# Optimization experiments

Measured on AMD Instinct MI355X. Metric: run time of the kernel, lower is better.

Reference implementation:

```python
import jax, jax.numpy as jnp
import numpy as np

B, S, H, KVH, D, MD = 4, 4096, 2, 1, 2, 5  # batch, seq, heads, kv heads, head_dim, model_dim
EPS, SCALE = 1e-6, 16.0


def _rmsnorm(t):
    # RMSNormNoWeight with scale=16.0 over last dim
    var = jnp.mean(t * t, axis=-1, keepdims=True)
    return SCALE * t * jax.lax.rsqrt(var + EPS)


def _rope(t, cos, sin):
    # t: (B, S, h, D); cos/sin: (S, D//2). Complex multiply on interleaved pairs.
    tr, ti = t[..., 0::2], t[..., 1::2]
    c = cos[None, :, None, :]
    s = sin[None, :, None, :]
    out_r = tr * c - ti * s
    out_i = tr * s + ti * c
    return jnp.stack([out_r, out_i], axis=-1).reshape(t.shape)


def setup_inputs() -> dict:
    key = jax.random.key(0)
    ks = jax.random.split(key, 9)
    return {
        "x": jax.random.normal(ks[0], (B, S, MD), jnp.float32),
        "freqs": jax.random.normal(ks[1], (S, D // 2), jnp.float32),
        "shared_qk_v": jax.random.normal(ks[2], (MD,), jnp.float32),
        "shared_v_v": jax.random.normal(ks[3], (MD,), jnp.float32),
        "shared_o_v": jax.random.normal(ks[4], (H * D,), jnp.float32),
        "shared_vproj_u": jax.random.normal(ks[5], (KVH * D,), jnp.float32),
        "q_u": jax.random.normal(ks[6], (H * D,), jnp.float32),
        "k_u": jax.random.normal(ks[7], (KVH * D,), jnp.float32),
        "o_u": jax.random.normal(ks[8], (MD,), jnp.float32),
    }


def reference(x, freqs, shared_qk_v, shared_v_v, shared_o_v, shared_vproj_u, q_u, k_u, o_u):
    b, s = x.shape[0], x.shape[1]
    # rank-1 projections: (x . v) outer u
    s_qk = jnp.sum(x * shared_qk_v, axis=-1, keepdims=True)  # (B,S,1) shared by q and k
    q = (s_qk * q_u).reshape(b, s, H, D)
    k = (s_qk * k_u).reshape(b, s, KVH, D)
    s_v = jnp.sum(x * shared_v_v, axis=-1, keepdims=True)
    v = (s_v * shared_vproj_u).reshape(b, s, KVH, D)
    # qk-norm + rotary
    q = _rmsnorm(q)
    k = _rmsnorm(k)
    cos, sin = jnp.cos(freqs), jnp.sin(freqs)
    q = _rope(q, cos, sin)
    k = _rope(k, cos, sin)
    # (B,h,S,D)
    q = q.transpose(0, 2, 1, 3)
    k = k.transpose(0, 2, 1, 3)
    v = v.transpose(0, 2, 1, 3)
    # GQA repeat kv heads
    k = jnp.repeat(k, H // KVH, axis=1)
    v = jnp.repeat(v, H // KVH, axis=1)
    scores = jnp.einsum('bhqd,bhkd->bhqk', q, k) / jnp.sqrt(jnp.float32(D))
    probs = jax.nn.softmax(scores, axis=-1)
    out = jnp.einsum('bhqk,bhkd->bhqd', probs, v)
    out = out.transpose(0, 2, 1, 3).reshape(b, s, H * D)
    # rank-1 output projection
    s_o = jnp.sum(out * shared_o_v, axis=-1, keepdims=True)
    return s_o * o_u  # (B,S,MODEL_DIM)
```

## Files before the change

kernel.cpp:

```cpp
#include <hip/hip_runtime.h>
#include <math.h>


#define BQ 4
#define SQ 4096
#define MDQ 5
#define EPSQ 1e-6f
#define SCALEQ 16.0f
#define L2E 1.4426950408889634f
#define ISQ2 0.70710678118654752f

typedef float v2f __attribute__((ext_vector_type(2)));

__device__ __forceinline__ float fast_exp2(float x) {
#if __has_builtin(__builtin_amdgcn_exp2f)
    return __builtin_amdgcn_exp2f(x);
#else
    return __expf(x * 0.6931471805599453f);
#endif
}

__global__ __launch_bounds__(256)
void ca_prep(const float* __restrict__ x, const float* __restrict__ freqs,
             const float* __restrict__ qk_v, const float* __restrict__ v_v,
             const float* __restrict__ k_u, float4* __restrict__ pqc)
{
    const int idx = blockIdx.x * 256 + threadIdx.x;
    const int j   = idx & (SQ - 1);

    const float w0 = k_u[0], w1 = k_u[1];
    const float mk = 0.5f * (w0 * w0 + w1 * w1);

    const float qk0 = qk_v[0], qk1 = qk_v[1], qk2 = qk_v[2], qk3 = qk_v[3], qk4 = qk_v[4];
    const float vv0 = v_v[0],  vv1 = v_v[1],  vv2 = v_v[2],  vv3 = v_v[3],  vv4 = v_v[4];

    const float* xr = x + (size_t)idx * MDQ;
    const float x0 = xr[0], x1 = xr[1], x2 = xr[2], x3 = xr[3], x4 = xr[4];
    const float a  = x0*qk0 + x1*qk1 + x2*qk2 + x3*qk3 + x4*qk4;
    const float sv = x0*vv0 + x1*vv1 + x2*vv2 + x3*vv3 + x4*vv4;

    float sj, cj;
    __sincosf(freqs[j], &sj, &cj);
    const float mu = SCALEQ * a * rsqrtf(a * a * mk + EPSQ);
    pqc[idx] = make_float4(mu * cj, mu * sj, sv, sv);
}

#define BLOCK 256
#define RSETS 4
#define RPT 2
#define ROWSB (RSETS * RPT)
#define TILES (SQ / ROWSB)
#define KTILE 256
#define NKT (SQ / KTILE)
#define JPT (KTILE / 64)

__global__ __launch_bounds__(BLOCK)
void ca_main(const float* __restrict__ x,
             const float* __restrict__ freqs,
             const float* __restrict__ qk_v,
             const float* __restrict__ o_v,
             const float* __restrict__ vproj_u,
             const float* __restrict__ q_u,
             const float* __restrict__ k_u,
             const float* __restrict__ o_u,
             const float4* __restrict__ pqc,
             float* __restrict__ out)
{
    __shared__ float4 sKey[2][KTILE];

    const int tid = threadIdx.x;
    const int sp  = tid & 63;
    const int rs  = tid >> 6;
    const int bx  = blockIdx.x;
    const int b   = bx / TILES;
    const int tile = bx % TILES;
    const int i0  = tile * ROWSB + rs * RPT;

    const float w0 = k_u[0], w1 = k_u[1];
    const float mk  = 0.5f * (w0 * w0 + w1 * w1);
    const float Mmu = SCALEQ * rsqrtf(mk);

    const float qk0 = qk_v[0], qk1 = qk_v[1], qk2 = qk_v[2], qk3 = qk_v[3], qk4 = qk_v[4];
    const float u00 = q_u[0], u01 = q_u[1], u10 = q_u[2], u11 = q_u[3];
    const float m0 = 0.5f * (u00 * u00 + u01 * u01);
    const float m1 = 0.5f * (u10 * u10 + u11 * u11);
    const float A0 = u00 * w0 + u01 * w1, B0 = u01 * w0 - u00 * w1;
    const float A1 = u10 * w0 + u11 * w1, B1 = u11 * w0 - u10 * w1;

    v2f al[RPT], be[RPT], Cc[RPT];
#pragma unroll
    for (int k = 0; k < RPT; ++k) {
        const int i = i0 + k;
        const float* xi = x + (size_t)(b * SQ + i) * MDQ;
        const float ai = xi[0]*qk0 + xi[1]*qk1 + xi[2]*qk2 + xi[3]*qk3 + xi[4]*qk4;
        float si, ci;
        __sincosf(freqs[i], &si, &ci);
        const float lam0 = SCALEQ * ai * rsqrtf(ai * ai * m0 + EPSQ);
        const float lam1 = SCALEQ * ai * rsqrtf(ai * ai * m1 + EPSQ);
        const float a0  = lam0 * (A0 * ci - B0 * si) * ISQ2;
        const float b0_ = lam0 * (A0 * si + B0 * ci) * ISQ2;
        const float a1  = lam1 * (A1 * ci - B1 * si) * ISQ2;
        const float b1_ = lam1 * (A1 * si + B1 * ci) * ISQ2;
        const float r0 = sqrtf(a0 * a0 + b0_ * b0_);
        const float r1 = sqrtf(a1 * a1 + b1_ * b1_);
        al[k] = (v2f){a0 * L2E, a1 * L2E};
        be[k] = (v2f){b0_ * L2E, b1_ * L2E};
        Cc[k] = (v2f){-r0 * Mmu * L2E, -r1 * Mmu * L2E};
    }

    const float4* __restrict__ gsrc = pqc + (size_t)b * SQ + tid;

    float4 stage = gsrc[0];
    sKey[0][tid] = stage;
    __syncthreads();

    v2f l[RPT], n[RPT];
#pragma unroll
    for (int k = 0; k < RPT; ++k) { l[k] = (v2f){0.f, 0.f}; n[k] = (v2f){0.f, 0.f}; }

    for (int t = 0; t < NKT; ++t) {
        const int cur = t & 1;
        if (t + 1 < NKT) stage = gsrc[(size_t)(t + 1) * KTILE];

        const float4* kb = &sKey[cur][sp];
#pragma unroll
        for (int jj = 0; jj < JPT; ++jj) {
            const float4 v = kb[jj * 64];
            const v2f vx = (v2f){v.x, v.x};
            const v2f vy = (v2f){v.y, v.y};
            const v2f vz = (v2f){v.z, v.w};
#pragma unroll
            for (int k = 0; k < RPT; ++k) {
                const v2f s = al[k] * vx + (be[k] * vy + Cc[k]);
                v2f e;
                e.x = fast_exp2(s.x);
                e.y = fast_exp2(s.y);
                l[k] += e;
                n[k] += e * vz;
            }
        }

        if (t + 1 < NKT) {
            sKey[cur ^ 1][tid] = stage;
            __syncthreads();
        }
    }

#pragma unroll
    for (int m = 1; m < 64; m <<= 1) {
#pragma unroll
        for (int k = 0; k < RPT; ++k) {
            l[k].x += __shfl_xor(l[k].x, m, 64);
            l[k].y += __shfl_xor(l[k].y, m, 64);
            n[k].x += __shfl_xor(n[k].x, m, 64);
            n[k].y += __shfl_xor(n[k].y, m, 64);
        }
    }

    if (sp < RPT) {
        const int k = sp;
        const float L0 = fmaxf(l[k].x, 1e-30f);
        const float L1 = fmaxf(l[k].y, 1e-30f);
        const float W0 = n[k].x / L0, W1 = n[k].y / L1;

        const float p0 = vproj_u[0], p1 = vproj_u[1];
        const float d0 = p0 * o_v[0] + p1 * o_v[1];
        const float d1 = p0 * o_v[2] + p1 * o_v[3];
        const float so = W0 * d0 + W1 * d1;

        float* orow = out + (size_t)(b * SQ + i0 + k) * MDQ;
        orow[0] = so * o_u[0];
        orow[1] = so * o_u[1];
        orow[2] = so * o_u[2];
        orow[3] = so * o_u[3];
        orow[4] = so * o_u[4];
    }
}

#define FROWS 32
#define FSPLIT 8
#define FJSUB (SQ / FSPLIT)
#define FTILES (SQ / FROWS)

__global__ __launch_bounds__(256)
void ca_fallback(const float* __restrict__ x,
                 const float* __restrict__ freqs,
                 const float* __restrict__ qk_v,
                 const float* __restrict__ v_v,
                 const float* __restrict__ o_v,
                 const float* __restrict__ vproj_u,
                 const float* __restrict__ q_u,
                 const float* __restrict__ k_u,
                 const float* __restrict__ o_u,
                 float* __restrict__ out)
{
    __shared__ float2 sPQ[SQ];
    __shared__ float  sCv[SQ];
    __shared__ float4 sRed[FROWS][FSPLIT];

    const int tid  = threadIdx.x;
    const int b    = blockIdx.x / FTILES;
    const int tile = blockIdx.x % FTILES;

    const float w0 = k_u[0], w1 = k_u[1];
    const float mk  = 0.5f * (w0 * w0 + w1 * w1);
    const float Mmu = SCALEQ * rsqrtf(mk);

    const float qk0 = qk_v[0], qk1 = qk_v[1], qk2 = qk_v[2], qk3 = qk_v[3], qk4 = qk_v[4];
    const float vv0 = v_v[0],  vv1 = v_v[1],  vv2 = v_v[2],  vv3 = v_v[3],  vv4 = v_v[4];

    for (int k = 0; k < SQ / 256; ++k) {
        const int j = tid + k * 256;
        const float* xr = x + (size_t)(b * SQ + j) * MDQ;
        const float x0 = xr[0], x1 = xr[1], x2 = xr[2], x3 = xr[3], x4 = xr[4];
        const float a  = x0*qk0 + x1*qk1 + x2*qk2 + x3*qk3 + x4*qk4;
        const float sv = x0*vv0 + x1*vv1 + x2*vv2 + x3*vv3 + x4*vv4;
        float sj, cj;
        __sincosf(freqs[j], &sj, &cj);
        const float mu = SCALEQ * a * rsqrtf(a * a * mk + EPSQ);
        sPQ[j] = make_float2(mu * cj, mu * sj);
        sCv[j] = sv;
    }

    const int row = tid & (FROWS - 1);
    const int sp  = tid / FROWS;
    const int i   = tile * FROWS + row;

    const float u00 = q_u[0], u01 = q_u[1], u10 = q_u[2], u11 = q_u[3];
    const float m0 = 0.5f * (u00 * u00 + u01 * u01);
    const float m1 = 0.5f * (u10 * u10 + u11 * u11);
    const float A0 = u00 * w0 + u01 * w1, B0 = u01 * w0 - u00 * w1;
    const float A1 = u10 * w0 + u11 * w1, B1 = u11 * w0 - u10 * w1;

    const float* xi = x + (size_t)(b * SQ + i) * MDQ;
    const float ai = xi[0]*qk0 + xi[1]*qk1 + xi[2]*qk2 + xi[3]*qk3 + xi[4]*qk4;
    float si, ci;
    __sincosf(freqs[i], &si, &ci);
    const float lam0 = SCALEQ * ai * rsqrtf(ai * ai * m0 + EPSQ);
    const float lam1 = SCALEQ * ai * rsqrtf(ai * ai * m1 + EPSQ);
    const float alr0 = lam0 * (A0 * ci - B0 * si) * ISQ2;
    const float ber0 = lam0 * (A0 * si + B0 * ci) * ISQ2;
    const float alr1 = lam1 * (A1 * ci - B1 * si) * ISQ2;
    const float ber1 = lam1 * (A1 * si + B1 * ci) * ISQ2;
    const float r0 = sqrtf(alr0 * alr0 + ber0 * ber0);
    const float r1 = sqrtf(alr1 * alr1 + ber1 * ber1);
    const float al0 = alr0 * L2E, be0 = ber0 * L2E, C0 = -r0 * Mmu * L2E;
    const float al1 = alr1 * L2E, be1 = ber1 * L2E, C1 = -r1 * Mmu * L2E;

    __syncthreads();

    const float2* __restrict__ pq  = sPQ + sp * FJSUB;
    const float*  __restrict__ cvp = sCv + sp * FJSUB;
    float l0 = 0.f, n0 = 0.f, l1 = 0.f, n1 = 0.f;
#pragma unroll 8
    for (int jj = 0; jj < FJSUB; ++jj) {
        const float2 v = pq[jj];
        const float cv = cvp[jj];
        const float s0 = fmaf(al0, v.x, fmaf(be0, v.y, C0));
        const float s1 = fmaf(al1, v.x, fmaf(be1, v.y, C1));
        const float e0 = fast_exp2(s0);
        const float e1 = fast_exp2(s1);
        l0 += e0; n0 = fmaf(e0, cv, n0);
        l1 += e1; n1 = fmaf(e1, cv, n1);
    }

    sRed[row][sp] = make_float4(l0, n0, l1, n1);
    __syncthreads();

    if (tid < FROWS) {
        float L0 = 0.f, N0 = 0.f, L1 = 0.f, N1 = 0.f;
#pragma unroll
        for (int s = 0; s < FSPLIT; ++s) {
            const float4 t = sRed[tid][s];
            L0 += t.x; N0 += t.y; L1 += t.z; N1 += t.w;
        }
        L0 = fmaxf(L0, 1e-30f);
        L1 = fmaxf(L1, 1e-30f);
        const float W0 = N0 / L0, W1 = N1 / L1;
        const float p0 = vproj_u[0], p1 = vproj_u[1];
        const float d0 = p0 * o_v[0] + p1 * o_v[1];
        const float d1 = p0 * o_v[2] + p1 * o_v[3];
        const float so = W0 * d0 + W1 * d1;

        const int ig = tile * FROWS + tid;
        float* orow = out + (size_t)(b * SQ + ig) * MDQ;
        orow[0] = so * o_u[0];
        orow[1] = so * o_u[1];
        orow[2] = so * o_u[2];
        orow[3] = so * o_u[3];
        orow[4] = so * o_u[4];
    }
}

extern "C" void kernel_launch(void* const* d_in, const int* in_sizes, int n_in,
                              void* d_out, int out_size, void* d_ws, size_t ws_size,
                              hipStream_t stream) {
    (void)in_sizes; (void)n_in; (void)out_size;
    const float* x       = (const float*)d_in[0];
    const float* freqs   = (const float*)d_in[1];
    const float* qk_v    = (const float*)d_in[2];
    const float* v_v     = (const float*)d_in[3];
    const float* o_v     = (const float*)d_in[4];
    const float* vproj_u = (const float*)d_in[5];
    const float* q_u     = (const float*)d_in[6];
    const float* k_u     = (const float*)d_in[7];
    const float* o_u     = (const float*)d_in[8];
    float* out = (float*)d_out;

    const size_t pqc_bytes = (size_t)BQ * SQ * sizeof(float4);
    if (ws_size >= pqc_bytes) {
        float4* pqc = (float4*)d_ws;
        hipLaunchKernelGGL(ca_prep, dim3(BQ * SQ / 256), dim3(256), 0, stream,
                           x, freqs, qk_v, v_v, k_u, pqc);
        hipLaunchKernelGGL(ca_main, dim3(BQ * TILES), dim3(BLOCK), 0, stream,
                           x, freqs, qk_v, o_v, vproj_u, q_u, k_u, o_u, pqc, out);
    } else {
        hipLaunchKernelGGL(ca_fallback, dim3(BQ * FTILES), dim3(256), 0, stream,
                           x, freqs, qk_v, v_v, o_v, vproj_u, q_u, k_u, o_u, out);
    }
}
```

Baseline: 92.92 us.

## Split key workspace into packed float2/float arrays and double key tile size

The prep kernel now writes the rotated key pair and the value scalar to two separate arrays instead of one padded float4 with a duplicated value. The main kernel stages 512 keys per tile, loading two keys per float4 and two values per float2, so each thread handles two keys per shared-memory read. It also adds a min-blocks hint to launch_bounds. This cuts workspace and global/LDS traffic per key by a quarter and halves the number of tile barriers, at the cost of more registers per iteration, which the occupancy hint may constrain.

```diff
diff --git a/kernel.cpp b/kernel.cpp
--- a/kernel.cpp
+++ b/kernel.cpp
@@ -23,7 +23,8 @@
 __global__ __launch_bounds__(256)
 void ca_prep(const float* __restrict__ x, const float* __restrict__ freqs,
              const float* __restrict__ qk_v, const float* __restrict__ v_v,
-             const float* __restrict__ k_u, float4* __restrict__ pqc)
+             const float* __restrict__ k_u,
+             float2* __restrict__ pq2, float* __restrict__ cv)
 {
     const int idx = blockIdx.x * 256 + threadIdx.x;
     const int j   = idx & (SQ - 1);
@@ -42,7 +43,8 @@
     float sj, cj;
     __sincosf(freqs[j], &sj, &cj);
     const float mu = SCALEQ * a * rsqrtf(a * a * mk + EPSQ);
-    pqc[idx] = make_float4(mu * cj, mu * sj, sv, sv);
+    pq2[idx] = make_float2(mu * cj, mu * sj);
+    cv[idx]  = sv;
 }
 
 #define BLOCK 256
@@ -50,11 +52,11 @@
 #define RPT 2
 #define ROWSB (RSETS * RPT)
 #define TILES (SQ / ROWSB)
-#define KTILE 256
+#define KTILE 512
 #define NKT (SQ / KTILE)
-#define JPT (KTILE / 64)
-
-__global__ __launch_bounds__(BLOCK)
+#define PAIRS (KTILE / 128)
+
+__global__ __launch_bounds__(BLOCK, 8)
 void ca_main(const float* __restrict__ x,
              const float* __restrict__ freqs,
              const float* __restrict__ qk_v,
@@ -63,10 +65,12 @@
              const float* __restrict__ q_u,
              const float* __restrict__ k_u,
              const float* __restrict__ o_u,
-             const float4* __restrict__ pqc,
+             const float2* __restrict__ pq2,
+             const float* __restrict__ cv,
              float* __restrict__ out)
 {
-    __shared__ float4 sKey[2][KTILE];
+    __shared__ float4 sPQ[2][KTILE / 2];
+    __shared__ float2 sCv[2][KTILE / 2];
 
     const int tid = threadIdx.x;
     const int sp  = tid & 63;
@@ -108,10 +112,13 @@
         Cc[k] = (v2f){-r0 * Mmu * L2E, -r1 * Mmu * L2E};
     }
 
-    const float4* __restrict__ gsrc = pqc + (size_t)b * SQ + tid;
-
-    float4 stage = gsrc[0];
-    sKey[0][tid] = stage;
+    const float4* __restrict__ gPQ = (const float4*)(pq2 + (size_t)b * SQ) + tid;
+    const float2* __restrict__ gCv = (const float2*)(cv  + (size_t)b * SQ) + tid;
+
+    float4 stPQ = gPQ[0];
+    float2 stCv = gCv[0];
+    sPQ[0][tid] = stPQ;
+    sCv[0][tid] = stCv;
     __syncthreads();
 
     v2f l[RPT], n[RPT];
@@ -120,28 +127,33 @@
 
     for (int t = 0; t < NKT; ++t) {
         const int cur = t & 1;
-        if (t + 1 < NKT) stage = gsrc[(size_t)(t + 1) * KTILE];
-
-        const float4* kb = &sKey[cur][sp];
-#pragma unroll
-        for (int jj = 0; jj < JPT; ++jj) {
-            const float4 v = kb[jj * 64];
-            const v2f vx = (v2f){v.x, v.x};
-            const v2f vy = (v2f){v.y, v.y};
-            const v2f vz = (v2f){v.z, v.w};
+        if (t + 1 < NKT) {
+            stPQ = gPQ[(size_t)(t + 1) * (KTILE / 2)];
+            stCv = gCv[(size_t)(t + 1) * (KTILE / 2)];
+        }
+
+#pragma unroll
+        for (int jj = 0; jj < PAIRS; ++jj) {
+            const float4 pq = sPQ[cur][jj * 64 + sp];
+            const float2 cw = sCv[cur][jj * 64 + sp];
+
+            const v2f vx0 = (v2f){pq.x, pq.x}, vy0 = (v2f){pq.y, pq.y}, vz0 = (v2f){cw.x, cw.x};
+            const v2f vx1 = (v2f){pq.z, pq.z}, vy1 = (v2f){pq.w, pq.w}, vz1 = (v2f){cw.y, cw.y};
 #pragma unroll
             for (int k = 0; k < RPT; ++k) {
-                const v2f s = al[k] * vx + (be[k] * vy + Cc[k]);
-                v2f e;
-                e.x = fast_exp2(s.x);
-                e.y = fast_exp2(s.y);
-                l[k] += e;
-                n[k] += e * vz;
+                const v2f s0 = al[k] * vx0 + (be[k] * vy0 + Cc[k]);
+                const v2f s1 = al[k] * vx1 + (be[k] * vy1 + Cc[k]);
+                v2f e0, e1;
+                e0.x = fast_exp2(s0.x);  e0.y = fast_exp2(s0.y);
+                e1.x = fast_exp2(s1.x);  e1.y = fast_exp2(s1.y);
+                l[k] += e0 + e1;
+                n[k] += e0 * vz0 + e1 * vz1;
             }
         }
 
         if (t + 1 < NKT) {
-            sKey[cur ^ 1][tid] = stage;
+            sPQ[cur ^ 1][tid] = stPQ;
+            sCv[cur ^ 1][tid] = stCv;
             __syncthreads();
         }
     }
@@ -255,13 +267,13 @@
 #pragma unroll 8
     for (int jj = 0; jj < FJSUB; ++jj) {
         const float2 v = pq[jj];
-        const float cv = cvp[jj];
+        const float cvx = cvp[jj];
         const float s0 = fmaf(al0, v.x, fmaf(be0, v.y, C0));
         const float s1 = fmaf(al1, v.x, fmaf(be1, v.y, C1));
         const float e0 = fast_exp2(s0);
         const float e1 = fast_exp2(s1);
-        l0 += e0; n0 = fmaf(e0, cv, n0);
-        l1 += e1; n1 = fmaf(e1, cv, n1);
+        l0 += e0; n0 = fmaf(e0, cvx, n0);
+        l1 += e1; n1 = fmaf(e1, cvx, n1);
     }
 
     sRed[row][sp] = make_float4(l0, n0, l1, n1);
@@ -307,13 +319,15 @@
     const float* o_u     = (const float*)d_in[8];
     float* out = (float*)d_out;
 
-    const size_t pqc_bytes = (size_t)BQ * SQ * sizeof(float4);
-    if (ws_size >= pqc_bytes) {
-        float4* pqc = (float4*)d_ws;
+    const size_t pq_bytes = (size_t)BQ * SQ * sizeof(float2);
+    const size_t cv_bytes = (size_t)BQ * SQ * sizeof(float);
+    if (ws_size >= pq_bytes + cv_bytes) {
+        float2* pq2 = (float2*)d_ws;
+        float*  cvp = (float*)((char*)d_ws + pq_bytes);
         hipLaunchKernelGGL(ca_prep, dim3(BQ * SQ / 256), dim3(256), 0, stream,
-                           x, freqs, qk_v, v_v, k_u, pqc);
+                           x, freqs, qk_v, v_v, k_u, pq2, cvp);
         hipLaunchKernelGGL(ca_main, dim3(BQ * TILES), dim3(BLOCK), 0, stream,
-                           x, freqs, qk_v, o_v, vproj_u, q_u, k_u, o_u, pqc, out);
+                           x, freqs, qk_v, o_v, vproj_u, q_u, k_u, o_u, pq2, cvp, out);
     } else {
         hipLaunchKernelGGL(ca_fallback, dim3(BQ * FTILES), dim3(256), 0, stream,
                            x, freqs, qk_v, v_v, o_v, vproj_u, q_u, k_u, o_u, out);
```

After: 94.85 us. +2.1%, slower.

## Split key workspace into SoA planes and vectorize over keys instead of heads

Applied to the files above, without the earlier changes.

The prep kernel now writes three separate float planes (P, Q, C) instead of one padded float4 per key, cutting the redundant duplicated value channel. The main kernel loads a larger key tile, reads float4 groups of four consecutive keys from each plane, and packs two keys per packed-math op with per-head scalars broadcast, giving more independent accumulators. This is meant to raise ALU and LDS efficiency in the exp-bound inner loop, at the cost of more registers and three shared arrays.

```diff
diff --git a/kernel.cpp b/kernel.cpp
--- a/kernel.cpp
+++ b/kernel.cpp
@@ -23,7 +23,8 @@
 __global__ __launch_bounds__(256)
 void ca_prep(const float* __restrict__ x, const float* __restrict__ freqs,
              const float* __restrict__ qk_v, const float* __restrict__ v_v,
-             const float* __restrict__ k_u, float4* __restrict__ pqc)
+             const float* __restrict__ k_u,
+             float* __restrict__ pP, float* __restrict__ pQ, float* __restrict__ pC)
 {
     const int idx = blockIdx.x * 256 + threadIdx.x;
     const int j   = idx & (SQ - 1);
@@ -42,7 +43,9 @@
     float sj, cj;
     __sincosf(freqs[j], &sj, &cj);
     const float mu = SCALEQ * a * rsqrtf(a * a * mk + EPSQ);
-    pqc[idx] = make_float4(mu * cj, mu * sj, sv, sv);
+    pP[idx] = mu * cj;
+    pQ[idx] = mu * sj;
+    pC[idx] = sv;
 }
 
 #define BLOCK 256
@@ -50,9 +53,9 @@
 #define RPT 2
 #define ROWSB (RSETS * RPT)
 #define TILES (SQ / ROWSB)
-#define KTILE 256
+#define KTILE 512
 #define NKT (SQ / KTILE)
-#define JPT (KTILE / 64)
+#define NCOMBO (RPT * 2)
 
 __global__ __launch_bounds__(BLOCK)
 void ca_main(const float* __restrict__ x,
@@ -63,10 +66,14 @@
              const float* __restrict__ q_u,
              const float* __restrict__ k_u,
              const float* __restrict__ o_u,
-             const float4* __restrict__ pqc,
+             const float* __restrict__ pP,
+             const float* __restrict__ pQ,
+             const float* __restrict__ pC,
              float* __restrict__ out)
 {
-    __shared__ float4 sKey[2][KTILE];
+    __shared__ float sP[2][KTILE];
+    __shared__ float sQ[2][KTILE];
+    __shared__ float sC[2][KTILE];
 
     const int tid = threadIdx.x;
     const int sp  = tid & 63;
@@ -87,7 +94,7 @@
     const float A0 = u00 * w0 + u01 * w1, B0 = u01 * w0 - u00 * w1;
     const float A1 = u10 * w0 + u11 * w1, B1 = u11 * w0 - u10 * w1;
 
-    v2f al[RPT], be[RPT], Cc[RPT];
+    v2f alS[NCOMBO], beS[NCOMBO], CS[NCOMBO];
 #pragma unroll
     for (int k = 0; k < RPT; ++k) {
         const int i = i0 + k;
@@ -103,45 +110,58 @@
         const float b1_ = lam1 * (A1 * si + B1 * ci) * ISQ2;
         const float r0 = sqrtf(a0 * a0 + b0_ * b0_);
         const float r1 = sqrtf(a1 * a1 + b1_ * b1_);
-        al[k] = (v2f){a0 * L2E, a1 * L2E};
-        be[k] = (v2f){b0_ * L2E, b1_ * L2E};
-        Cc[k] = (v2f){-r0 * Mmu * L2E, -r1 * Mmu * L2E};
-    }
-
-    const float4* __restrict__ gsrc = pqc + (size_t)b * SQ + tid;
-
-    float4 stage = gsrc[0];
-    sKey[0][tid] = stage;
+        const float A0l = a0 * L2E,  B0l = b0_ * L2E,  C0l = -r0 * Mmu * L2E;
+        const float A1l = a1 * L2E,  B1l = b1_ * L2E,  C1l = -r1 * Mmu * L2E;
+        alS[2*k+0] = (v2f){A0l, A0l};  beS[2*k+0] = (v2f){B0l, B0l};  CS[2*k+0] = (v2f){C0l, C0l};
+        alS[2*k+1] = (v2f){A1l, A1l};  beS[2*k+1] = (v2f){B1l, B1l};  CS[2*k+1] = (v2f){C1l, C1l};
+    }
+
+    const float2* __restrict__ gP2 = (const float2*)(pP + (size_t)b * SQ);
+    const float2* __restrict__ gQ2 = (const float2*)(pQ + (size_t)b * SQ);
+    const float2* __restrict__ gC2 = (const float2*)(pC + (size_t)b * SQ);
+
+    float2 stP = gP2[tid], stQ = gQ2[tid], stC = gC2[tid];
+    ((float2*)sP[0])[tid] = stP;
+    ((float2*)sQ[0])[tid] = stQ;
+    ((float2*)sC[0])[tid] = stC;
     __syncthreads();
 
-    v2f l[RPT], n[RPT];
-#pragma unroll
-    for (int k = 0; k < RPT; ++k) { l[k] = (v2f){0.f, 0.f}; n[k] = (v2f){0.f, 0.f}; }
+    v2f l[NCOMBO], n[NCOMBO];
+#pragma unroll
+    for (int c = 0; c < NCOMBO; ++c) { l[c] = (v2f){0.f, 0.f}; n[c] = (v2f){0.f, 0.f}; }
 
     for (int t = 0; t < NKT; ++t) {
         const int cur = t & 1;
-        if (t + 1 < NKT) stage = gsrc[(size_t)(t + 1) * KTILE];
-
-        const float4* kb = &sKey[cur][sp];
-#pragma unroll
-        for (int jj = 0; jj < JPT; ++jj) {
-            const float4 v = kb[jj * 64];
-            const v2f vx = (v2f){v.x, v.x};
-            const v2f vy = (v2f){v.y, v.y};
-            const v2f vz = (v2f){v.z, v.w};
-#pragma unroll
-            for (int k = 0; k < RPT; ++k) {
-                const v2f s = al[k] * vx + (be[k] * vy + Cc[k]);
-                v2f e;
-                e.x = fast_exp2(s.x);
-                e.y = fast_exp2(s.y);
-                l[k] += e;
-                n[k] += e * vz;
+        if (t + 1 < NKT) {
+            const int e = (t + 1) * (KTILE / 2) + tid;
+            stP = gP2[e];  stQ = gQ2[e];  stC = gC2[e];
+        }
+
+#pragma unroll
+        for (int jj = 0; jj < KTILE / 256; ++jj) {
+            const int idx = jj * 64 + sp;
+            const float4 P4 = ((const float4*)sP[cur])[idx];
+            const float4 Q4 = ((const float4*)sQ[cur])[idx];
+            const float4 C4 = ((const float4*)sC[cur])[idx];
+            const v2f p01 = (v2f){P4.x, P4.y}, p23 = (v2f){P4.z, P4.w};
+            const v2f q01 = (v2f){Q4.x, Q4.y}, q23 = (v2f){Q4.z, Q4.w};
+            const v2f c01 = (v2f){C4.x, C4.y}, c23 = (v2f){C4.z, C4.w};
+#pragma unroll
+            for (int c = 0; c < NCOMBO; ++c) {
+                const v2f s01 = alS[c] * p01 + (beS[c] * q01 + CS[c]);
+                const v2f s23 = alS[c] * p23 + (beS[c] * q23 + CS[c]);
+                v2f e01, e23;
+                e01.x = fast_exp2(s01.x);  e01.y = fast_exp2(s01.y);
+                e23.x = fast_exp2(s23.x);  e23.y = fast_exp2(s23.y);
+                l[c] += e01;  l[c] += e23;
+                n[c] += e01 * c01;  n[c] += e23 * c23;
             }
         }
 
         if (t + 1 < NKT) {
-            sKey[cur ^ 1][tid] = stage;
+            ((float2*)sP[cur ^ 1])[tid] = stP;
+            ((float2*)sQ[cur ^ 1])[tid] = stQ;
+            ((float2*)sC[cur ^ 1])[tid] = stC;
             __syncthreads();
         }
     }
@@ -149,19 +169,21 @@
 #pragma unroll
     for (int m = 1; m < 64; m <<= 1) {
 #pragma unroll
-        for (int k = 0; k < RPT; ++k) {
-            l[k].x += __shfl_xor(l[k].x, m, 64);
-            l[k].y += __shfl_xor(l[k].y, m, 64);
-            n[k].x += __shfl_xor(n[k].x, m, 64);
-            n[k].y += __shfl_xor(n[k].y, m, 64);
+        for (int c = 0; c < NCOMBO; ++c) {
+            l[c].x += __shfl_xor(l[c].x, m, 64);
+            l[c].y += __shfl_xor(l[c].y, m, 64);
+            n[c].x += __shfl_xor(n[c].x, m, 64);
+            n[c].y += __shfl_xor(n[c].y, m, 64);
         }
     }
 
     if (sp < RPT) {
         const int k = sp;
-        const float L0 = fmaxf(l[k].x, 1e-30f);
-        const float L1 = fmaxf(l[k].y, 1e-30f);
-        const float W0 = n[k].x / L0, W1 = n[k].y / L1;
+        const float L0 = fmaxf(l[2*k+0].x + l[2*k+0].y, 1e-30f);
+        const float L1 = fmaxf(l[2*k+1].x + l[2*k+1].y, 1e-30f);
+        const float N0 = n[2*k+0].x + n[2*k+0].y;
+        const float N1 = n[2*k+1].x + n[2*k+1].y;
+        const float W0 = N0 / L0, W1 = N1 / L1;
 
         const float p0 = vproj_u[0], p1 = vproj_u[1];
         const float d0 = p0 * o_v[0] + p1 * o_v[1];
@@ -255,13 +277,13 @@
 #pragma unroll 8
     for (int jj = 0; jj < FJSUB; ++jj) {
         const float2 v = pq[jj];
-        const float cv = cvp[jj];
+        const float cvx = cvp[jj];
         const float s0 = fmaf(al0, v.x, fmaf(be0, v.y, C0));
         const float s1 = fmaf(al1, v.x, fmaf(be1, v.y, C1));
         const float e0 = fast_exp2(s0);
         const float e1 = fast_exp2(s1);
-        l0 += e0; n0 = fmaf(e0, cv, n0);
-        l1 += e1; n1 = fmaf(e1, cv, n1);
+        l0 += e0; n0 = fmaf(e0, cvx, n0);
+        l1 += e1; n1 = fmaf(e1, cvx, n1);
     }
 
     sRed[row][sp] = make_float4(l0, n0, l1, n1);
@@ -307,13 +329,15 @@
     const float* o_u     = (const float*)d_in[8];
     float* out = (float*)d_out;
 
-    const size_t pqc_bytes = (size_t)BQ * SQ * sizeof(float4);
-    if (ws_size >= pqc_bytes) {
-        float4* pqc = (float4*)d_ws;
+    const size_t plane = (size_t)BQ * SQ;
+    if (ws_size >= 3 * plane * sizeof(float)) {
+        float* pP = (float*)d_ws;
+        float* pQ = pP + plane;
+        float* pC = pQ + plane;
         hipLaunchKernelGGL(ca_prep, dim3(BQ * SQ / 256), dim3(256), 0, stream,
-                           x, freqs, qk_v, v_v, k_u, pqc);
+                           x, freqs, qk_v, v_v, k_u, pP, pQ, pC);
         hipLaunchKernelGGL(ca_main, dim3(BQ * TILES), dim3(BLOCK), 0, stream,
-                           x, freqs, qk_v, o_v, vproj_u, q_u, k_u, o_u, pqc, out);
+                           x, freqs, qk_v, o_v, vproj_u, q_u, k_u, o_u, pP, pQ, pC, out);
     } else {
         hipLaunchKernelGGL(ca_fallback, dim3(BQ * FTILES), dim3(256), 0, stream,
                            x, freqs, qk_v, v_v, o_v, vproj_u, q_u, k_u, o_u, out);
```

After: 96.04 us. +3.4%, slower.
